# Kernel optimization log

Measured on AMD Instinct MI355X. Metric: run time of the kernel, lower is better.

## Reference

```python
import jax, jax.numpy as jnp
import numpy as np

H, C, PQ, PV = 12, 16, 4, 8  # heads, scalar head dim, query points, value points
EPS = 1e-8


def setup_inputs() -> dict:
    key = jax.random.key(0)
    ks = jax.random.split(key, 16)
    B, N, S, Z = 2, 512, 384, 128
    def w(k, fan_in, shape):
        return jax.random.normal(k, shape, jnp.float32) / np.sqrt(fan_in)
    return {
        's': jax.random.normal(ks[0], (B, N, S), jnp.float32),
        'z': jax.random.normal(ks[1], (B, N, N, Z), jnp.float32),
        'R': jax.random.normal(ks[2], (B, N, 3, 3), jnp.float32),
        't': jax.random.normal(ks[3], (B, N, 3), jnp.float32),
        'Wq': w(ks[4], S, (S, H * C)),
        'Wk': w(ks[5], S, (S, H * C)),
        'Wv': w(ks[6], S, (S, H * C)),
        'Wqp': w(ks[7], S, (S, H * PQ * 3)),
        'Wkp': w(ks[8], S, (S, H * PQ * 3)),
        'Wvp': w(ks[9], S, (S, H * PV * 3)),
        'Wb': w(ks[10], Z, (Z, H)),
        'head_weights': jax.random.normal(ks[11], (H,), jnp.float32) * 0.1,
        'Wout': w(ks[12], H * (C + 4 * PV + Z), (H * (C + 4 * PV + Z), S)),
    }


def reference(s, z, R, t, Wq, Wk, Wv, Wqp, Wkp, Wvp, Wb, head_weights, Wout):
    B, N, _ = s.shape
    Zc = z.shape[-1]
    # scalar q/k/v: [B,N,H,C]
    q = (s @ Wq).reshape(B, N, H, C)
    k = (s @ Wk).reshape(B, N, H, C)
    v = (s @ Wv).reshape(B, N, H, C)
    # point q/k/v in local frames, then map to global: x_g = R x + t
    def to_global(Wp, P):
        p = (s @ Wp).reshape(B, N, H, P, 3)
        return jnp.einsum('bnxy,bnhpy->bnhpx', R, p) + t[:, :, None, None, :]
    qp = to_global(Wqp, PQ)   # [B,N,H,PQ,3]
    kp = to_global(Wkp, PQ)
    vp = to_global(Wvp, PV)   # [B,N,H,PV,3]
    # pair bias [B,H,N,N]
    b = jnp.einsum('bijz,zh->bhij', z, Wb)
    # scalar attention logits
    scal = jnp.einsum('bihc,bjhc->bhij', q, k) / np.sqrt(C)
    # squared point distances via expansion (avoid [B,N,N,H,PQ,3] tensor)
    qq = jnp.sum(qp * qp, axis=(-1, -2))                    # [B,N,H]
    kk = jnp.sum(kp * kp, axis=(-1, -2))                    # [B,N,H]
    qk = jnp.einsum('bihpx,bjhpx->bhij', qp, kp)
    dist2 = qq.transpose(0, 2, 1)[:, :, :, None] + kk.transpose(0, 2, 1)[:, :, None, :] - 2.0 * qk
    gamma = jax.nn.softplus(head_weights)                   # [H]
    wC = np.sqrt(2.0 / (9.0 * PQ))
    wL = np.sqrt(1.0 / 3.0)
    logits = wL * (scal + b) - (wL * wC / 2.0) * gamma[None, :, None, None] * dist2
    a = jax.nn.softmax(logits, axis=-1)                     # [B,H,N,N]
    # scalar output
    o = jnp.einsum('bhij,bjhc->bihc', a, v).reshape(B, N, H * C)
    # point output: aggregate in global frame, then back to local: R^T (x - t)
    opt_g = jnp.einsum('bhij,bjhpx->bihpx', a, vp)
    d = opt_g - t[:, :, None, None, :]
    opt = jnp.einsum('bnyx,bnhpy->bnhpx', R, d)             # R^T d
    opt_norm = jnp.sqrt(jnp.sum(opt * opt, axis=-1) + EPS)  # [B,N,H,PV]
    # pair output
    opair = jnp.einsum('bhij,bijz->bihz', a, z).reshape(B, N, H * Zc)
    cat = jnp.concatenate([o, opt.reshape(B, N, H * PV * 3),
                           opt_norm.reshape(B, N, H * PV), opair], axis=-1)
    return cat @ Wout
```

## Files before the change

kernel.cpp:

```cpp
#include <hip/hip_runtime.h>
#include <math.h>

#define BB 2
#define NN 512
#define SDIM 384
#define ZDIM 128
#define HH 12
#define CDIM 16
#define PQ 4
#define PV 8
#define BN (BB*NN)
#define CATD 2112

#define WL  0.57735026918962576f
#define LAM 0.06804138174397717f

#define OFF_Q    0
#define OFF_QP   196608
#define OFF_QQ   344064
#define OFF_KT4  356352
#define OFF_KPT4 552960
#define OFF_KKT  700416
#define OFF_V    712704
#define OFF_VP   909312
#define OFF_CAT  7495680

__device__ __forceinline__ float dot4(float4 a, float4 b) {
    return a.x*b.x + a.y*b.y + a.z*b.z + a.w*b.w;
}
__device__ __forceinline__ void fma4(float4& a, float s, float4 b) {
    a.x += s*b.x; a.y += s*b.y; a.z += s*b.z; a.w += s*b.w;
}
__device__ __forceinline__ void add4(float4& a, float4 b) {
    a.x += b.x; a.y += b.y; a.z += b.z; a.w += b.w;
}
__device__ __forceinline__ void mul4(float4& a, float s) {
    a.x *= s; a.y *= s; a.z *= s; a.w *= s;
}

__global__ __launch_bounds__(256) void k_proj(
    const float* __restrict__ s, const float* __restrict__ Rg, const float* __restrict__ tg,
    const float* __restrict__ Wq, const float* __restrict__ Wk, const float* __restrict__ Wv,
    const float* __restrict__ Wqp, const float* __restrict__ Wkp, const float* __restrict__ Wvp,
    float* __restrict__ ws)
{
    __shared__ float4 pL4[2][144];
    __shared__ float  sqL[2][96];
    __shared__ float  Rt[2][12];
    const int t = threadIdx.x;
    const int n0 = blockIdx.x * 2;
    const int b  = n0 >> 9;
    const int nloc = n0 & 511;

    if (t < 24) {
        int rr = t / 12, c = t % 12;
        Rt[rr][c] = (c < 9) ? Rg[(n0+rr)*9 + c] : tg[(n0+rr)*3 + (c-9)];
    }
    const float* s0 = s + (size_t)n0*SDIM;
    const float* s1 = s0 + SDIM;
    __syncthreads();

    float4* Q4g  = (float4*)(ws + OFF_Q);
    float4* V4g  = (float4*)(ws + OFF_V);
    float4* KT4g = (float4*)(ws + OFF_KT4);

    for (int it = 0; it < 2; ++it) {
        int g = t + it*256;
        if (g >= 288) break;
        const float4* W4; int wc4, ld4, dst;
        if (g < 48)       { W4 = (const float4*)Wq;  wc4 = g;     ld4 = 48; dst = 0; }
        else if (g < 96)  { W4 = (const float4*)Wk;  wc4 = g-48;  ld4 = 48; dst = 1; }
        else if (g < 144) { W4 = (const float4*)Wv;  wc4 = g-96;  ld4 = 48; dst = 2; }
        else if (g < 180) { W4 = (const float4*)Wqp; wc4 = g-144; ld4 = 36; dst = 3; }
        else if (g < 216) { W4 = (const float4*)Wkp; wc4 = g-180; ld4 = 36; dst = 4; }
        else              { W4 = (const float4*)Wvp; wc4 = g-216; ld4 = 72; dst = 5; }
        float4 acc0 = {0,0,0,0}, acc1 = {0,0,0,0};
        #pragma unroll 4
        for (int r = 0; r < SDIM; ++r) {
            float4 wv = W4[r*ld4 + wc4];
            float f0 = s0[r], f1 = s1[r];
            fma4(acc0, f0, wv);
            fma4(acc1, f1, wv);
        }
        if (dst == 0) {
            Q4g[(size_t)n0*48 + wc4] = acc0;
            Q4g[(size_t)(n0+1)*48 + wc4] = acc1;
        } else if (dst == 1) {
            size_t base = ((size_t)(b*48 + wc4))*512 + nloc;
            KT4g[base] = acc0; KT4g[base+1] = acc1;
        } else if (dst == 2) {
            V4g[(size_t)n0*48 + wc4] = acc0;
            V4g[(size_t)(n0+1)*48 + wc4] = acc1;
        } else if (dst == 3) {
            pL4[0][wc4] = acc0; pL4[1][wc4] = acc1;
        } else if (dst == 4) {
            pL4[0][36+wc4] = acc0; pL4[1][36+wc4] = acc1;
        } else {
            pL4[0][72+wc4] = acc0; pL4[1][72+wc4] = acc1;
        }
    }
    __syncthreads();

    for (int task = t; task < 384; task += 256) {
        int rr = task / 192, pt = task % 192;
        const float* pl = (const float*)pL4[rr];
        int off = (pt < 48) ? pt*3 : (pt < 96 ? 144 + (pt-48)*3 : 288 + (pt-96)*3);
        float p0 = pl[off], p1 = pl[off+1], p2 = pl[off+2];
        const float* R = Rt[rr];
        float g0 = R[0]*p0 + R[1]*p1 + R[2]*p2 + R[9];
        float g1 = R[3]*p0 + R[4]*p1 + R[5]*p2 + R[10];
        float g2 = R[6]*p0 + R[7]*p1 + R[8]*p2 + R[11];
        int bn = n0 + rr, n = bn & 511;
        if (pt < 48) {
            int o = pt*3;
            float* d = ws + OFF_QP + (size_t)bn*144 + o;
            d[0] = g0; d[1] = g1; d[2] = g2;
            sqL[rr][pt] = g0*g0 + g1*g1 + g2*g2;
        } else if (pt < 96) {
            int pc = (pt-48)*3;
            float gg[3] = {g0,g1,g2};
            #pragma unroll
            for (int x = 0; x < 3; ++x) {
                int pcx = pc + x;
                ws[OFF_KPT4 + (((size_t)(b*36 + (pcx>>2)))*512 + n)*4 + (pcx&3)] = gg[x];
            }
            sqL[rr][pt] = g0*g0 + g1*g1 + g2*g2;
        } else {
            int o = (pt-96)*3;
            float* d = ws + OFF_VP + (size_t)bn*288 + o;
            d[0] = g0; d[1] = g1; d[2] = g2;
        }
    }
    __syncthreads();

    if (t < 48) {
        int rr = t / 24, u = t % 24;
        int bn = n0 + rr, n = bn & 511;
        if (u < 12) {
            float sm = sqL[rr][u*4] + sqL[rr][u*4+1] + sqL[rr][u*4+2] + sqL[rr][u*4+3];
            ws[OFF_QQ + (size_t)bn*12 + u] = sm;
        } else {
            int h = u - 12;
            float sm = sqL[rr][48+h*4] + sqL[rr][48+h*4+1] + sqL[rr][48+h*4+2] + sqL[rr][48+h*4+3];
            ws[OFF_KKT + ((size_t)(b*12 + h))*512 + n] = sm;
        }
    }
}

__global__ __launch_bounds__(512, 2) void k_attn(
    const float* __restrict__ z, const float* __restrict__ Rg, const float* __restrict__ tg,
    const float* __restrict__ hw, const float* __restrict__ Wb, float* __restrict__ ws)
{
    __shared__ __align__(16) float aL[HH*516];
    __shared__ float4 optgS4[72];
    __shared__ float RiL[9], tiL[3], sInv[12];

    const int t = threadIdx.x;
    const int d = blockIdx.x;
    const int xcd = d & 7, slot = d >> 3;
    const int bi = (xcd < 4) ? (xcd*128 + slot) : (512 + (xcd-4)*128 + slot);
    const int b = bi >> 9;

    if (t < 9)             RiL[t]   = Rg[bi*9 + t];
    if (t >= 9 && t < 12)  tiL[t-9] = tg[bi*3 + (t-9)];

    float gam[HH];
    #pragma unroll
    for (int h = 0; h < HH; ++h) {
        float x = hw[h];
        gam[h] = (x > 20.f) ? x : log1pf(__expf(x));
    }

    {
        const int j = t;
        float pb[HH];
        #pragma unroll
        for (int h = 0; h < HH; ++h) pb[h] = 0.f;
        const float4* zrow4 = (const float4*)z + ((size_t)bi*512 + j)*32;
        #pragma unroll 4
        for (int c4 = 0; c4 < 32; ++c4) {
            const float4 zq = zrow4[c4];
            const float* wb = Wb + c4*48;
            #pragma unroll
            for (int e = 0; e < 4; ++e) {
                const float zv = ((const float*)&zq)[e];
                const float* w = wb + e*12;
                #pragma unroll
                for (int h = 0; h < HH; ++h) pb[h] += zv * w[h];
            }
        }
        const float4* Q4u  = (const float4*)(ws + OFF_Q  + (size_t)bi*192);
        const float4* QP4u = (const float4*)(ws + OFF_QP + (size_t)bi*144);
        const float*  QQu  = ws + OFF_QQ + (size_t)bi*12;
        const float4* KT4  = (const float4*)(ws + OFF_KT4)  + (size_t)b*48*512;
        const float4* KPT4 = (const float4*)(ws + OFF_KPT4) + (size_t)b*36*512;
        const float*  KKT  = ws + OFF_KKT  + (size_t)b*12*512;
        for (int h = 0; h < HH; ++h) {
            float scal = 0.f, qk = 0.f;
            #pragma unroll
            for (int cg = 0; cg < 4; ++cg)
                scal += dot4(Q4u[h*4+cg], KT4[(h*4+cg)*512 + j]);
            #pragma unroll
            for (int pg = 0; pg < 3; ++pg)
                qk += dot4(QP4u[h*3+pg], KPT4[(h*3+pg)*512 + j]);
            float dist2 = QQu[h] + KKT[h*512 + j] - 2.f*qk;
            aL[h*516 + j] = WL*(scal*0.25f + pb[h]) - LAM*gam[h]*dist2;
        }
    }
    __syncthreads();

    {
        const int w = t >> 6, lane = t & 63;
        for (int h = w; h < HH; h += 8) {
            float* row = aL + h*516;
            float m = -1e30f;
            #pragma unroll
            for (int k = 0; k < 8; ++k) m = fmaxf(m, row[lane + 64*k]);
            #pragma unroll
            for (int off = 32; off > 0; off >>= 1) m = fmaxf(m, __shfl_xor(m, off));
            float ssum = 0.f;
            #pragma unroll
            for (int k = 0; k < 8; ++k) {
                float e = __expf(row[lane + 64*k] - m);
                row[lane + 64*k] = e;
                ssum += e;
            }
            #pragma unroll
            for (int off = 32; off > 0; off >>= 1) ssum += __shfl_xor(ssum, off);
            if (lane == 0) sInv[h] = 1.f / ssum;
        }
    }
    __syncthreads();

    float4 acc0 = {0,0,0,0}, acc1 = {0,0,0,0}, acc2 = {0,0,0,0};
    int rid = -1, seg = 0;

#define FMA8(ZB, AP0, AP1, AP2, JT) do { \
    float4 av0 = *(const float4*)((AP0) + (JT)); \
    float4 av1 = *(const float4*)((AP1) + (JT)); \
    float4 av2 = *(const float4*)((AP2) + (JT)); \
    float4 aw0 = *(const float4*)((AP0) + (JT) + 4); \
    float4 aw1 = *(const float4*)((AP1) + (JT) + 4); \
    float4 aw2 = *(const float4*)((AP2) + (JT) + 4); \
    fma4(acc0, av0.x, ZB[0]); fma4(acc1, av1.x, ZB[0]); fma4(acc2, av2.x, ZB[0]); \
    fma4(acc0, av0.y, ZB[1]); fma4(acc1, av1.y, ZB[1]); fma4(acc2, av2.y, ZB[1]); \
    fma4(acc0, av0.z, ZB[2]); fma4(acc1, av1.z, ZB[2]); fma4(acc2, av2.z, ZB[2]); \
    fma4(acc0, av0.w, ZB[3]); fma4(acc1, av1.w, ZB[3]); fma4(acc2, av2.w, ZB[3]); \
    fma4(acc0, aw0.x, ZB[4]); fma4(acc1, aw1.x, ZB[4]); fma4(acc2, aw2.x, ZB[4]); \
    fma4(acc0, aw0.y, ZB[5]); fma4(acc1, aw1.y, ZB[5]); fma4(acc2, aw2.y, ZB[5]); \
    fma4(acc0, aw0.z, ZB[6]); fma4(acc1, aw1.z, ZB[6]); fma4(acc2, aw2.z, ZB[6]); \
    fma4(acc0, aw0.w, ZB[7]); fma4(acc1, aw1.w, ZB[7]); fma4(acc2, aw2.w, ZB[7]); \
} while (0)

    if (t < 384) {
        seg = t >> 7;
        rid = t & 127;
        const int hg = rid >> 5, zc4 = rid & 31;
        const int j0 = seg*176;
        const int ngrp = (seg == 2) ? 20 : 22;
        const float4* Zp = (const float4*)z + (size_t)bi*512*32 + zc4;
        const float* a0p = aL + hg*516;
        const float* a1p = aL + (hg+4)*516;
        const float* a2p = aL + (hg+8)*516;
        float4 zA[8], zB[8];
        #pragma unroll
        for (int e = 0; e < 8; ++e) zA[e] = Zp[(size_t)(j0+e)*32];
        for (int p = 0; p < ngrp; p += 2) {
            const int jt = j0 + p*8;
            #pragma unroll
            for (int e = 0; e < 8; ++e) zB[e] = Zp[(size_t)(jt+8+e)*32];
            FMA8(zA, a0p, a1p, a2p, jt);
            if (p + 2 < ngrp) {
                #pragma unroll
                for (int e = 0; e < 8; ++e) zA[e] = Zp[(size_t)(jt+16+e)*32];
            }
            FMA8(zB, a0p, a1p, a2p, jt + 8);
        }
    } else if (t < 504) {
        const int v = t - 384;
        seg = v / 40;
        const int w = v % 40;
        rid = 128 + w;
        const int j0 = seg*176, j1 = (seg == 2) ? 512 : j0 + 176;
        const float4* P; int S, D, O, hg;
        if (w < 16) {
            hg = w >> 2; S = 48; D = 16; O = hg*4 + (w & 3);
            P = (const float4*)(ws + OFF_V) + (size_t)b*512*48;
        } else {
            const int v2 = w - 16;
            hg = v2 / 6; S = 72; D = 24; O = hg*6 + v2 % 6;
            P = (const float4*)(ws + OFF_VP) + (size_t)b*512*72;
        }
        const float* a0p = aL + hg*516;
        const float* a1p = aL + (hg+4)*516;
        const float* a2p = aL + (hg+8)*516;
        #pragma unroll 2
        for (int jt = j0; jt < j1; jt += 4) {
            float4 av0 = *(const float4*)(a0p + jt);
            float4 av1 = *(const float4*)(a1p + jt);
            float4 av2 = *(const float4*)(a2p + jt);
            #pragma unroll
            for (int e = 0; e < 4; ++e) {
                const size_t base = (size_t)(jt+e)*S + O;
                fma4(acc0, ((const float*)&av0)[e], P[base]);
                fma4(acc1, ((const float*)&av1)[e], P[base + D]);
                fma4(acc2, ((const float*)&av2)[e], P[base + 2*D]);
            }
        }
    }
    __syncthreads();
    float4* sc4 = (float4*)aL;
    if (rid >= 0) {
        const int si = (seg*168 + rid)*3;
        sc4[si] = acc0; sc4[si+1] = acc1; sc4[si+2] = acc2;
    }
    __syncthreads();

    if (t < 168) {
        float4 r0 = {0,0,0,0}, r1 = {0,0,0,0}, r2 = {0,0,0,0};
        #pragma unroll
        for (int ss = 0; ss < 3; ++ss) {
            const int si = (ss*168 + t)*3;
            add4(r0, sc4[si]); add4(r1, sc4[si+1]); add4(r2, sc4[si+2]);
        }
        int typ, hg;
        if (t < 128)      { typ = 0; hg = t >> 5; }
        else if (t < 144) { typ = 1; hg = (t-128) >> 2; }
        else              { typ = 2; hg = (t-144) / 6; }
        mul4(r0, sInv[hg]); mul4(r1, sInv[hg+4]); mul4(r2, sInv[hg+8]);
        float4* cat4 = (float4*)(ws + OFF_CAT);
        const size_t cb = (size_t)bi * 528;
        if (typ == 0) {
            const int zc4 = t & 31;
            cat4[cb + 144 + (hg  )*32 + zc4] = r0;
            cat4[cb + 144 + (hg+4)*32 + zc4] = r1;
            cat4[cb + 144 + (hg+8)*32 + zc4] = r2;
        } else if (typ == 1) {
            const int c4 = (t-128) & 3;
            cat4[cb + (hg  )*4 + c4] = r0;
            cat4[cb + (hg+4)*4 + c4] = r1;
            cat4[cb + (hg+8)*4 + c4] = r2;
        } else {
            const int po = (t-144) % 6;
            optgS4[(hg  )*6 + po] = r0;
            optgS4[(hg+4)*6 + po] = r1;
            optgS4[(hg+8)*6 + po] = r2;
        }
    }
    __syncthreads();

    if (t < 96) {
        const float* og = (const float*)optgS4;
        int h = t >> 3, p = t & 7;
        int o = h*24 + p*3;
        float d0 = og[o]   - tiL[0];
        float d1 = og[o+1] - tiL[1];
        float d2 = og[o+2] - tiL[2];
        float ox = RiL[0]*d0 + RiL[3]*d1 + RiL[6]*d2;
        float oy = RiL[1]*d0 + RiL[4]*d1 + RiL[7]*d2;
        float oz = RiL[2]*d0 + RiL[5]*d1 + RiL[8]*d2;
        float* cat = ws + OFF_CAT + (size_t)bi*CATD;
        cat[192 + o]     = ox;
        cat[192 + o + 1] = oy;
        cat[192 + o + 2] = oz;
        cat[480 + h*8 + p] = sqrtf(ox*ox + oy*oy + oz*oz + 1e-8f);
    }
}

__global__ __launch_bounds__(384) void k_out(
    const float* __restrict__ Wout, const float* __restrict__ ws, float* __restrict__ out)
{
    __shared__ __align__(16) float catS[4*CATD];
    const int t = threadIdx.x;
    const int row0 = blockIdx.x * 4;
    {
        const float4* src = (const float4*)(ws + OFF_CAT + (size_t)row0*CATD);
        float4* dst = (float4*)catS;
        #pragma unroll
        for (int i = t; i < 4*528; i += 384) dst[i] = src[i];
    }
    __syncthreads();
    const float* c0 = catS;
    const float* c1 = catS + CATD;
    const float* c2 = catS + 2*CATD;
    const float* c3 = catS + 3*CATD;
    float a0 = 0.f, a1 = 0.f, a2 = 0.f, a3 = 0.f;
    #pragma unroll 8
    for (int r = 0; r < CATD; ++r) {
        float w = Wout[(size_t)r*384 + t];
        a0 += c0[r]*w; a1 += c1[r]*w; a2 += c2[r]*w; a3 += c3[r]*w;
    }
    out[(size_t)(row0+0)*384 + t] = a0;
    out[(size_t)(row0+1)*384 + t] = a1;
    out[(size_t)(row0+2)*384 + t] = a2;
    out[(size_t)(row0+3)*384 + t] = a3;
}

extern "C" void kernel_launch(void* const* d_in, const int* in_sizes, int n_in,
                              void* d_out, int out_size, void* d_ws, size_t ws_size,
                              hipStream_t stream)
{
    const float* s    = (const float*)d_in[0];
    const float* z    = (const float*)d_in[1];
    const float* R    = (const float*)d_in[2];
    const float* tt   = (const float*)d_in[3];
    const float* Wq   = (const float*)d_in[4];
    const float* Wk   = (const float*)d_in[5];
    const float* Wv   = (const float*)d_in[6];
    const float* Wqp  = (const float*)d_in[7];
    const float* Wkp  = (const float*)d_in[8];
    const float* Wvp  = (const float*)d_in[9];
    const float* Wb   = (const float*)d_in[10];
    const float* hw   = (const float*)d_in[11];
    const float* Wout = (const float*)d_in[12];
    float* ws  = (float*)d_ws;
    float* out = (float*)d_out;

    hipLaunchKernelGGL(k_proj, dim3(BN/2), dim3(256), 0, stream,
                       s, R, tt, Wq, Wk, Wv, Wqp, Wkp, Wvp, ws);
    hipLaunchKernelGGL(k_attn, dim3(BN),   dim3(512), 0, stream, z, R, tt, hw, Wb, ws);
    hipLaunchKernelGGL(k_out,  dim3(BN/4), dim3(384), 0, stream, Wout, ws, out);
}
```

Measured before the change: 742.6 us.

## Halve z-load threads by having each accumulate six heads, rebalance value threads

The pair-output loop now uses 192 threads, each accumulating six head accumulators per z float4 instead of three. Each z element loaded from global memory is therefore reused for twice as many heads, halving redundant z reads. The freed 320 threads split the scalar and point value aggregation into 8 segments of 64 keys. The shared scratch and the reduction step are reorganized to match, which raises register pressure in the z threads and lengthens their serial loop.

```diff
diff --git a/kernel.cpp b/kernel.cpp
--- a/kernel.cpp
+++ b/kernel.cpp
@@ -151,7 +151,7 @@
     const float* __restrict__ z, const float* __restrict__ Rg, const float* __restrict__ tg,
     const float* __restrict__ hw, const float* __restrict__ Wb, float* __restrict__ ws)
 {
-    __shared__ __align__(16) float aL[HH*516];
+    __shared__ __align__(16) float aL[8448];
     __shared__ float4 optgS4[72];
     __shared__ float RiL[9], tiL[3], sInv[12];
 
@@ -232,36 +232,48 @@
     }
     __syncthreads();
 
-    float4 acc0 = {0,0,0,0}, acc1 = {0,0,0,0}, acc2 = {0,0,0,0};
-    int rid = -1, seg = 0;
-
-#define FMA8(ZB, AP0, AP1, AP2, JT) do { \
-    float4 av0 = *(const float4*)((AP0) + (JT)); \
-    float4 av1 = *(const float4*)((AP1) + (JT)); \
-    float4 av2 = *(const float4*)((AP2) + (JT)); \
-    float4 aw0 = *(const float4*)((AP0) + (JT) + 4); \
-    float4 aw1 = *(const float4*)((AP1) + (JT) + 4); \
-    float4 aw2 = *(const float4*)((AP2) + (JT) + 4); \
-    fma4(acc0, av0.x, ZB[0]); fma4(acc1, av1.x, ZB[0]); fma4(acc2, av2.x, ZB[0]); \
-    fma4(acc0, av0.y, ZB[1]); fma4(acc1, av1.y, ZB[1]); fma4(acc2, av2.y, ZB[1]); \
-    fma4(acc0, av0.z, ZB[2]); fma4(acc1, av1.z, ZB[2]); fma4(acc2, av2.z, ZB[2]); \
-    fma4(acc0, av0.w, ZB[3]); fma4(acc1, av1.w, ZB[3]); fma4(acc2, av2.w, ZB[3]); \
-    fma4(acc0, aw0.x, ZB[4]); fma4(acc1, aw1.x, ZB[4]); fma4(acc2, aw2.x, ZB[4]); \
-    fma4(acc0, aw0.y, ZB[5]); fma4(acc1, aw1.y, ZB[5]); fma4(acc2, aw2.y, ZB[5]); \
-    fma4(acc0, aw0.z, ZB[6]); fma4(acc1, aw1.z, ZB[6]); fma4(acc2, aw2.z, ZB[6]); \
-    fma4(acc0, aw0.w, ZB[7]); fma4(acc1, aw1.w, ZB[7]); fma4(acc2, aw2.w, ZB[7]); \
+    float4 acc0={0,0,0,0}, acc1={0,0,0,0}, acc2={0,0,0,0};
+    float4 acc3={0,0,0,0}, acc4={0,0,0,0}, acc5={0,0,0,0};
+
+    if (t < 192) {
+        const int seg0 = t / 64;
+        const int r = t & 63;
+        const int q = r >> 5, zc4 = r & 31;
+        const int j0 = seg0*176;
+        const int ngrp = (seg0 == 2) ? 20 : 22;
+        const float4* Zp = (const float4*)z + (size_t)bi*512*32 + zc4;
+        const float* aA0 = aL + (q   )*516;
+        const float* aA1 = aL + (q+4 )*516;
+        const float* aA2 = aL + (q+8 )*516;
+        const float* aB0 = aL + (q+2 )*516;
+        const float* aB1 = aL + (q+6 )*516;
+        const float* aB2 = aL + (q+10)*516;
+
+#define FMA8_6(ZB, JT) do { \
+    float4 vA0 = *(const float4*)(aA0 + (JT)); float4 wA0 = *(const float4*)(aA0 + (JT) + 4); \
+    float4 vA1 = *(const float4*)(aA1 + (JT)); float4 wA1 = *(const float4*)(aA1 + (JT) + 4); \
+    float4 vA2 = *(const float4*)(aA2 + (JT)); float4 wA2 = *(const float4*)(aA2 + (JT) + 4); \
+    float4 vB0 = *(const float4*)(aB0 + (JT)); float4 wB0 = *(const float4*)(aB0 + (JT) + 4); \
+    float4 vB1 = *(const float4*)(aB1 + (JT)); float4 wB1 = *(const float4*)(aB1 + (JT) + 4); \
+    float4 vB2 = *(const float4*)(aB2 + (JT)); float4 wB2 = *(const float4*)(aB2 + (JT) + 4); \
+    fma4(acc0, vA0.x, ZB[0]); fma4(acc1, vA1.x, ZB[0]); fma4(acc2, vA2.x, ZB[0]); \
+    fma4(acc3, vB0.x, ZB[0]); fma4(acc4, vB1.x, ZB[0]); fma4(acc5, vB2.x, ZB[0]); \
+    fma4(acc0, vA0.y, ZB[1]); fma4(acc1, vA1.y, ZB[1]); fma4(acc2, vA2.y, ZB[1]); \
+    fma4(acc3, vB0.y, ZB[1]); fma4(acc4, vB1.y, ZB[1]); fma4(acc5, vB2.y, ZB[1]); \
+    fma4(acc0, vA0.z, ZB[2]); fma4(acc1, vA1.z, ZB[2]); fma4(acc2, vA2.z, ZB[2]); \
+    fma4(acc3, vB0.z, ZB[2]); fma4(acc4, vB1.z, ZB[2]); fma4(acc5, vB2.z, ZB[2]); \
+    fma4(acc0, vA0.w, ZB[3]); fma4(acc1, vA1.w, ZB[3]); fma4(acc2, vA2.w, ZB[3]); \
+    fma4(acc3, vB0.w, ZB[3]); fma4(acc4, vB1.w, ZB[3]); fma4(acc5, vB2.w, ZB[3]); \
+    fma4(acc0, wA0.x, ZB[4]); fma4(acc1, wA1.x, ZB[4]); fma4(acc2, wA2.x, ZB[4]); \
+    fma4(acc3, wB0.x, ZB[4]); fma4(acc4, wB1.x, ZB[4]); fma4(acc5, wB2.x, ZB[4]); \
+    fma4(acc0, wA0.y, ZB[5]); fma4(acc1, wA1.y, ZB[5]); fma4(acc2, wA2.y, ZB[5]); \
+    fma4(acc3, wB0.y, ZB[5]); fma4(acc4, wB1.y, ZB[5]); fma4(acc5, wB2.y, ZB[5]); \
+    fma4(acc0, wA0.z, ZB[6]); fma4(acc1, wA1.z, ZB[6]); fma4(acc2, wA2.z, ZB[6]); \
+    fma4(acc3, wB0.z, ZB[6]); fma4(acc4, wB1.z, ZB[6]); fma4(acc5, wB2.z, ZB[6]); \
+    fma4(acc0, wA0.w, ZB[7]); fma4(acc1, wA1.w, ZB[7]); fma4(acc2, wA2.w, ZB[7]); \
+    fma4(acc3, wB0.w, ZB[7]); fma4(acc4, wB1.w, ZB[7]); fma4(acc5, wB2.w, ZB[7]); \
 } while (0)
 
-    if (t < 384) {
-        seg = t >> 7;
-        rid = t & 127;
-        const int hg = rid >> 5, zc4 = rid & 31;
-        const int j0 = seg*176;
-        const int ngrp = (seg == 2) ? 20 : 22;
-        const float4* Zp = (const float4*)z + (size_t)bi*512*32 + zc4;
-        const float* a0p = aL + hg*516;
-        const float* a1p = aL + (hg+4)*516;
-        const float* a2p = aL + (hg+8)*516;
         float4 zA[8], zB[8];
         #pragma unroll
         for (int e = 0; e < 8; ++e) zA[e] = Zp[(size_t)(j0+e)*32];
@@ -269,19 +281,19 @@
             const int jt = j0 + p*8;
             #pragma unroll
             for (int e = 0; e < 8; ++e) zB[e] = Zp[(size_t)(jt+8+e)*32];
-            FMA8(zA, a0p, a1p, a2p, jt);
+            FMA8_6(zA, jt);
             if (p + 2 < ngrp) {
                 #pragma unroll
                 for (int e = 0; e < 8; ++e) zA[e] = Zp[(size_t)(jt+16+e)*32];
             }
-            FMA8(zB, a0p, a1p, a2p, jt + 8);
-        }
-    } else if (t < 504) {
-        const int v = t - 384;
-        seg = v / 40;
+            FMA8_6(zB, jt + 8);
+        }
+#undef FMA8_6
+    } else {
+        const int v = t - 192;
+        const int seg8 = v / 40;
         const int w = v % 40;
-        rid = 128 + w;
-        const int j0 = seg*176, j1 = (seg == 2) ? 512 : j0 + 176;
+        const int j0 = seg8*64, j1 = j0 + 64;
         const float4* P; int S, D, O, hg;
         if (w < 16) {
             hg = w >> 2; S = 48; D = 16; O = hg*4 + (w & 3);
@@ -310,41 +322,53 @@
     }
     __syncthreads();
     float4* sc4 = (float4*)aL;
-    if (rid >= 0) {
-        const int si = (seg*168 + rid)*3;
+    if (t < 192) {
+        const int si = t*6;
+        sc4[si]   = acc0; sc4[si+1] = acc1; sc4[si+2] = acc2;
+        sc4[si+3] = acc3; sc4[si+4] = acc4; sc4[si+5] = acc5;
+    } else {
+        const int si = 1152 + (t-192)*3;
         sc4[si] = acc0; sc4[si+1] = acc1; sc4[si+2] = acc2;
     }
     __syncthreads();
 
     if (t < 168) {
         float4 r0 = {0,0,0,0}, r1 = {0,0,0,0}, r2 = {0,0,0,0};
-        #pragma unroll
-        for (int ss = 0; ss < 3; ++ss) {
-            const int si = (ss*168 + t)*3;
-            add4(r0, sc4[si]); add4(r1, sc4[si+1]); add4(r2, sc4[si+2]);
-        }
-        int typ, hg;
-        if (t < 128)      { typ = 0; hg = t >> 5; }
-        else if (t < 144) { typ = 1; hg = (t-128) >> 2; }
-        else              { typ = 2; hg = (t-144) / 6; }
-        mul4(r0, sInv[hg]); mul4(r1, sInv[hg+4]); mul4(r2, sInv[hg+8]);
         float4* cat4 = (float4*)(ws + OFF_CAT);
         const size_t cb = (size_t)bi * 528;
-        if (typ == 0) {
-            const int zc4 = t & 31;
+        if (t < 128) {
+            const int hg = t >> 5, zc4 = t & 31;
+            const int q = hg & 1, half = hg >> 1;
+            #pragma unroll
+            for (int ss = 0; ss < 3; ++ss) {
+                const int si = (ss*64 + q*32 + zc4)*6 + half*3;
+                add4(r0, sc4[si]); add4(r1, sc4[si+1]); add4(r2, sc4[si+2]);
+            }
+            mul4(r0, sInv[hg]); mul4(r1, sInv[hg+4]); mul4(r2, sInv[hg+8]);
             cat4[cb + 144 + (hg  )*32 + zc4] = r0;
             cat4[cb + 144 + (hg+4)*32 + zc4] = r1;
             cat4[cb + 144 + (hg+8)*32 + zc4] = r2;
-        } else if (typ == 1) {
-            const int c4 = (t-128) & 3;
-            cat4[cb + (hg  )*4 + c4] = r0;
-            cat4[cb + (hg+4)*4 + c4] = r1;
-            cat4[cb + (hg+8)*4 + c4] = r2;
         } else {
-            const int po = (t-144) % 6;
-            optgS4[(hg  )*6 + po] = r0;
-            optgS4[(hg+4)*6 + po] = r1;
-            optgS4[(hg+8)*6 + po] = r2;
+            const int w = t - 128;
+            #pragma unroll
+            for (int ss = 0; ss < 8; ++ss) {
+                const int si = 1152 + (ss*40 + w)*3;
+                add4(r0, sc4[si]); add4(r1, sc4[si+1]); add4(r2, sc4[si+2]);
+            }
+            if (w < 16) {
+                const int hg = w >> 2, c4 = w & 3;
+                mul4(r0, sInv[hg]); mul4(r1, sInv[hg+4]); mul4(r2, sInv[hg+8]);
+                cat4[cb + (hg  )*4 + c4] = r0;
+                cat4[cb + (hg+4)*4 + c4] = r1;
+                cat4[cb + (hg+8)*4 + c4] = r2;
+            } else {
+                const int v2 = w - 16;
+                const int hg = v2 / 6, po = v2 % 6;
+                mul4(r0, sInv[hg]); mul4(r1, sInv[hg+4]); mul4(r2, sInv[hg+8]);
+                optgS4[(hg  )*6 + po] = r0;
+                optgS4[(hg+4)*6 + po] = r1;
+                optgS4[(hg+8)*6 + po] = r2;
+            }
         }
     }
     __syncthreads();
```

After: 725.7 us (median of 3 runs). 2.3% less time.
